# Performance work log

Hardware: AMD Instinct MI355X
Metric: run time of the kernel (lower is better)

## Reference

```python
import jax, jax.numpy as jnp
import numpy as np

B, T, D, H = 4096, 512, 8, 64  # batch, seq_len, input_size, hidden_size


def setup_inputs() -> dict:
    key = jax.random.key(0)
    ks = jax.random.split(key, 11)
    s = lambda k, shape: (jax.random.normal(k, shape, dtype=jnp.float32) * 0.1)
    return {
        "x": jax.random.normal(ks[0], (B, T, D), dtype=jnp.float32),
        # layer 0 (input_size -> H), PyTorch gate order i,f,g,o packed along 4H
        "Wih0": s(ks[1], (4 * H, D)),
        "Whh0": s(ks[2], (4 * H, H)),
        "bih0": s(ks[3], (4 * H,)),
        "bhh0": s(ks[4], (4 * H,)),
        # layer 1 (H -> H)
        "Wih1": s(ks[5], (4 * H, H)),
        "Whh1": s(ks[6], (4 * H, H)),
        "bih1": s(ks[7], (4 * H,)),
        "bhh1": s(ks[8], (4 * H,)),
        # final linear head H -> 1
        "Wfc": s(ks[9], (1, H)),
        "bfc": s(ks[10], (1,)),
    }


def _lstm_layer(x, Wih, Whh, bih, bhh):
    """Single-direction LSTM layer over x:[B,T,Din] -> hs:[B,T,H]."""
    b, t, _ = x.shape
    h_dim = Whh.shape[1]
    # Precompute input contribution for all timesteps (one big GEMM).
    xg = jnp.einsum("btd,gd->btg", x, Wih) + bih + bhh  # [B,T,4H]

    def step(carry, gx_t):
        h, c = carry
        z = gx_t + h @ Whh.T  # [B,4H]
        i, f, g, o = jnp.split(z, 4, axis=-1)
        i = jax.nn.sigmoid(i)
        f = jax.nn.sigmoid(f)
        g = jnp.tanh(g)
        o = jax.nn.sigmoid(o)
        c = f * c + i * g
        h = o * jnp.tanh(c)
        return (h, c), h

    h0 = jnp.zeros((b, h_dim), x.dtype)
    c0 = jnp.zeros((b, h_dim), x.dtype)
    (_, _), hs = jax.lax.scan(step, (h0, c0), jnp.swapaxes(xg, 0, 1))
    return jnp.swapaxes(hs, 0, 1)  # [B,T,H]


def reference(x, Wih0, Whh0, bih0, bhh0, Wih1, Whh1, bih1, bhh1, Wfc, bfc):
    # nn.LSTM with num_layers=2, batch_first=True; dropout inactive in eval.
    h1 = _lstm_layer(x, Wih0, Whh0, bih0, bhh0)
    h2 = _lstm_layer(h1, Wih1, Whh1, bih1, bhh1)
    last = h2[:, -1, :]  # [B,H]
    return last @ Wfc.T + bfc  # [B,1]
```

## Files before the change

kernel.cpp:

```cpp
#include <hip/hip_runtime.h>

#define BTOT 4096
#define TB   512
#define BD   8
#define BSL  16

#define A0P1   2048
#define A1P0   8192
#define A1XOR  4096
#define S0     104
#define S1     136
#define LDSEL  16384

typedef __attribute__((ext_vector_type(8))) short  short8;
typedef __attribute__((ext_vector_type(4))) float  f32x4;

static __device__ __forceinline__ unsigned short f2bf(float f) {
    unsigned u = __float_as_uint(f);
    u += 0x7fffu + ((u >> 16) & 1u);
    return (unsigned short)(u >> 16);
}
static __device__ __forceinline__ float bf2f(unsigned short h) {
    return __uint_as_float(((unsigned)h) << 16);
}
static __device__ __forceinline__ float sigm(float x) {
    float e = __builtin_amdgcn_exp2f(-1.44269504f * x);
    return __builtin_amdgcn_rcpf(1.0f + e);
}
static __device__ __forceinline__ float tanh_(float x) {
    float e = __builtin_amdgcn_exp2f(2.88539008f * x);
    return 1.0f - 2.0f * __builtin_amdgcn_rcpf(1.0f + e);
}

template<int R0>
static __device__ __forceinline__ unsigned gates2(
    const f32x4 ai, const f32x4 af, const f32x4 ag, const f32x4 ao,
    float& c0, float& c1)
{
    float h0, h1;
    {
        const float iv = sigm(ai[R0]),     fv = sigm(af[R0]);
        const float gv = tanh_(ag[R0]),    ov = sigm(ao[R0]);
        c0 = fv * c0 + iv * gv;
        h0 = ov * tanh_(c0);
    }
    {
        const float iv = sigm(ai[R0 + 1]), fv = sigm(af[R0 + 1]);
        const float gv = tanh_(ag[R0 + 1]), ov = sigm(ao[R0 + 1]);
        c1 = fv * c1 + iv * gv;
        h1 = ov * tanh_(c1);
    }
    unsigned hp;
    asm("v_cvt_pk_bf16_f32 %0, %1, %2" : "=v"(hp) : "v"(h0), "v"(h1));
    return hp;
}

__global__ __launch_bounds__(1024) void lstm2_fused(
    const float* __restrict__ x,
    const float* __restrict__ Wih0, const float* __restrict__ Whh0,
    const float* __restrict__ bih0, const float* __restrict__ bhh0,
    const float* __restrict__ Wih1, const float* __restrict__ Whh1,
    const float* __restrict__ bih1, const float* __restrict__ bhh1,
    const float* __restrict__ Wfc,  const float* __restrict__ bfc,
    float* __restrict__ out)
{
    __shared__ __align__(16) unsigned short lds16[LDSEL];

    const int tid  = threadIdx.x;
    const int wid  = tid >> 6;
    const int lane = tid & 63;
    const int q    = lane >> 4;
    const int ln   = lane & 15;
    const int rb   = blockIdx.x * BSL;

    const bool L1w = (wid >= 8);
    const int  w   = L1w ? (wid - 8) : wid;
    const int  g   = w & 3;
    const int  rh  = w >> 2;
    const int  r0  = rh * 2;
    const int  jc  = g * 16 + ln;

    short8 Bf[4][4];
    #pragma unroll
    for (int G = 0; G < 4; ++G) {
        const int n = G * 64 + jc;
        #pragma unroll
        for (int ki = 0; ki < 4; ++ki) {
            union { unsigned short u[8]; short8 v; } t;
            #pragma unroll
            for (int j = 0; j < 8; ++j) {
                const int k = ki * 32 + q * 8 + j;
                float wv = 0.0f;
                if (!L1w) {
                    if (ki < 3) {
                        if (k < 64)      wv = Whh0[n * 64 + k];
                        else if (k < 72) wv = Wih0[n * 8 + (k - 64)];
                    }
                } else {
                    if (k < 64)          wv = Wih1[n * 64 + k];
                    else                 wv = Whh1[n * 64 + (k - 64)];
                }
                t.u[j] = f2bf(wv);
            }
            Bf[G][ki] = t.v;
        }
    }
    float bias[4];
    #pragma unroll
    for (int G = 0; G < 4; ++G) {
        const int n = G * 64 + jc;
        bias[G] = L1w ? (bih1[n] + bhh1[n]) : (bih0[n] + bhh0[n]);
    }

    {
        unsigned* z = (unsigned*)lds16;
        #pragma unroll
        for (int i = 0; i < 8; ++i) z[tid + i * 1024] = 0;
    }
    __syncthreads();

    const int xrow = g * 4 + (lane >> 1), xh = lane & 1;
    if (!L1w && rh == 0 && lane < 8) {
        const float4 v = *(const float4*)(x + ((size_t)(rb + xrow) * TB) * BD + xh * 4);
        unsigned p0, p1;
        asm("v_cvt_pk_bf16_f32 %0, %1, %2" : "=v"(p0) : "v"(v.x), "v"(v.y));
        asm("v_cvt_pk_bf16_f32 %0, %1, %2" : "=v"(p1) : "v"(v.z), "v"(v.w));
        *(uint2*)(lds16 + (xrow * S0 + 64 + xh * 4)) = make_uint2(p0, p1);
    }
    __syncthreads();

    int rdA, wrA, wrC = 0, wrX = 0, xrA, xrW;
    if (!L1w) {
        rdA = ln * S0 + q * 8;
        wrA = A0P1 + (q * 4 + r0) * S0 + jc;
        wrC = A1P0 + (q * 4 + r0) * S1 + jc;
        wrX = A0P1 + xrow * S0 + 64 + xh * 4;
        xrA = A0P1; xrW = A0P1;
    } else {
        rdA = A1P0 + A1XOR + ln * S1 + q * 8;
        wrA = A1P0 + (q * 4 + r0) * S1 + 64 + jc;
        xrA = A1XOR; xrW = A1XOR;
    }

    float cc0 = 0.f, cc1 = 0.f;

    for (int it = 0; it <= TB; ++it) {
        if (!L1w) {
            if (it < TB) {
                float4 xv;
                const bool dox = (rh == 0) && (lane < 8) && (it + 1 < TB);
                if (dox)
                    xv = *(const float4*)(x + ((size_t)(rb + xrow) * TB + (it + 1)) * BD + xh * 4);

                const short8 a0 = *(const short8*)(lds16 + rdA);
                const short8 a1 = *(const short8*)(lds16 + rdA + 32);
                const short8 a2 = *(const short8*)(lds16 + rdA + 64);

                f32x4 ai = {bias[0], bias[0], bias[0], bias[0]};
                f32x4 af = {bias[1], bias[1], bias[1], bias[1]};
                f32x4 ag = {bias[2], bias[2], bias[2], bias[2]};
                f32x4 ao = {bias[3], bias[3], bias[3], bias[3]};
                ai = __builtin_amdgcn_mfma_f32_16x16x32_bf16(a0, Bf[0][0], ai, 0, 0, 0);
                af = __builtin_amdgcn_mfma_f32_16x16x32_bf16(a0, Bf[1][0], af, 0, 0, 0);
                ag = __builtin_amdgcn_mfma_f32_16x16x32_bf16(a0, Bf[2][0], ag, 0, 0, 0);
                ao = __builtin_amdgcn_mfma_f32_16x16x32_bf16(a0, Bf[3][0], ao, 0, 0, 0);
                ai = __builtin_amdgcn_mfma_f32_16x16x32_bf16(a1, Bf[0][1], ai, 0, 0, 0);
                af = __builtin_amdgcn_mfma_f32_16x16x32_bf16(a1, Bf[1][1], af, 0, 0, 0);
                ag = __builtin_amdgcn_mfma_f32_16x16x32_bf16(a1, Bf[2][1], ag, 0, 0, 0);
                ao = __builtin_amdgcn_mfma_f32_16x16x32_bf16(a1, Bf[3][1], ao, 0, 0, 0);
                ai = __builtin_amdgcn_mfma_f32_16x16x32_bf16(a2, Bf[0][2], ai, 0, 0, 0);
                af = __builtin_amdgcn_mfma_f32_16x16x32_bf16(a2, Bf[1][2], af, 0, 0, 0);
                ag = __builtin_amdgcn_mfma_f32_16x16x32_bf16(a2, Bf[2][2], ag, 0, 0, 0);
                ao = __builtin_amdgcn_mfma_f32_16x16x32_bf16(a2, Bf[3][2], ao, 0, 0, 0);

                const unsigned hp = rh ? gates2<2>(ai, af, ag, ao, cc0, cc1)
                                       : gates2<0>(ai, af, ag, ao, cc0, cc1);
                lds16[wrA]      = (unsigned short)hp;
                lds16[wrA + S0] = (unsigned short)(hp >> 16);
                lds16[wrC]      = (unsigned short)hp;
                lds16[wrC + S1] = (unsigned short)(hp >> 16);

                if (dox) {
                    unsigned p0, p1;
                    asm("v_cvt_pk_bf16_f32 %0, %1, %2" : "=v"(p0) : "v"(xv.x), "v"(xv.y));
                    asm("v_cvt_pk_bf16_f32 %0, %1, %2" : "=v"(p1) : "v"(xv.z), "v"(xv.w));
                    *(uint2*)(lds16 + wrX) = make_uint2(p0, p1);
                }
            }
        } else {
            if (it >= 1) {
                const short8 a0 = *(const short8*)(lds16 + rdA);
                const short8 a1 = *(const short8*)(lds16 + rdA + 32);
                const short8 a2 = *(const short8*)(lds16 + rdA + 64);
                const short8 a3 = *(const short8*)(lds16 + rdA + 96);

                f32x4 ai = {bias[0], bias[0], bias[0], bias[0]};
                f32x4 af = {bias[1], bias[1], bias[1], bias[1]};
                f32x4 ag = {bias[2], bias[2], bias[2], bias[2]};
                f32x4 ao = {bias[3], bias[3], bias[3], bias[3]};
                ai = __builtin_amdgcn_mfma_f32_16x16x32_bf16(a0, Bf[0][0], ai, 0, 0, 0);
                af = __builtin_amdgcn_mfma_f32_16x16x32_bf16(a0, Bf[1][0], af, 0, 0, 0);
                ag = __builtin_amdgcn_mfma_f32_16x16x32_bf16(a0, Bf[2][0], ag, 0, 0, 0);
                ao = __builtin_amdgcn_mfma_f32_16x16x32_bf16(a0, Bf[3][0], ao, 0, 0, 0);
                ai = __builtin_amdgcn_mfma_f32_16x16x32_bf16(a1, Bf[0][1], ai, 0, 0, 0);
                af = __builtin_amdgcn_mfma_f32_16x16x32_bf16(a1, Bf[1][1], af, 0, 0, 0);
                ag = __builtin_amdgcn_mfma_f32_16x16x32_bf16(a1, Bf[2][1], ag, 0, 0, 0);
                ao = __builtin_amdgcn_mfma_f32_16x16x32_bf16(a1, Bf[3][1], ao, 0, 0, 0);
                ai = __builtin_amdgcn_mfma_f32_16x16x32_bf16(a2, Bf[0][2], ai, 0, 0, 0);
                af = __builtin_amdgcn_mfma_f32_16x16x32_bf16(a2, Bf[1][2], af, 0, 0, 0);
                ag = __builtin_amdgcn_mfma_f32_16x16x32_bf16(a2, Bf[2][2], ag, 0, 0, 0);
                ao = __builtin_amdgcn_mfma_f32_16x16x32_bf16(a2, Bf[3][2], ao, 0, 0, 0);
                ai = __builtin_amdgcn_mfma_f32_16x16x32_bf16(a3, Bf[0][3], ai, 0, 0, 0);
                af = __builtin_amdgcn_mfma_f32_16x16x32_bf16(a3, Bf[1][3], af, 0, 0, 0);
                ag = __builtin_amdgcn_mfma_f32_16x16x32_bf16(a3, Bf[2][3], ag, 0, 0, 0);
                ao = __builtin_amdgcn_mfma_f32_16x16x32_bf16(a3, Bf[3][3], ao, 0, 0, 0);

                const unsigned hp = rh ? gates2<2>(ai, af, ag, ao, cc0, cc1)
                                       : gates2<0>(ai, af, ag, ao, cc0, cc1);
                lds16[wrA]      = (unsigned short)hp;
                lds16[wrA + S1] = (unsigned short)(hp >> 16);
            }
        }
        __syncthreads();
        rdA ^= xrA; wrA ^= xrW; wrC ^= A1XOR; wrX ^= A0P1;
    }

    if (tid < BSL) {
        float s = bfc[0];
        #pragma unroll 8
        for (int j = 0; j < 64; ++j)
            s += bf2f(lds16[A1P0 + tid * S1 + 64 + j]) * Wfc[j];
        out[rb + tid] = s;
    }
}

extern "C" void kernel_launch(void* const* d_in, const int* in_sizes, int n_in,
                              void* d_out, int out_size, void* d_ws, size_t ws_size,
                              hipStream_t stream) {
    const float* x    = (const float*)d_in[0];
    const float* Wih0 = (const float*)d_in[1];
    const float* Whh0 = (const float*)d_in[2];
    const float* bih0 = (const float*)d_in[3];
    const float* bhh0 = (const float*)d_in[4];
    const float* Wih1 = (const float*)d_in[5];
    const float* Whh1 = (const float*)d_in[6];
    const float* bih1 = (const float*)d_in[7];
    const float* bhh1 = (const float*)d_in[8];
    const float* Wfc  = (const float*)d_in[9];
    const float* bfc  = (const float*)d_in[10];
    float* out = (float*)d_out;

    dim3 grid(BTOT / BSL);
    dim3 block(1024);
    lstm2_fused<<<grid, block, 0, stream>>>(x, Wih0, Whh0, bih0, bhh0,
                                            Wih1, Whh1, bih1, bhh1, Wfc, bfc, out);
}
```

Baseline: 607.5 us.

## Halve block to 512 threads, batch gate transcendentals, restage x and h layout

Each wave now covers all four accumulator rows, so a block uses 8 waves instead of 16 and two blocks can share a CU. The sigmoid and tanh scale factors are folded into the bf16 weights and biases. Reciprocals are batched with a product-tree trick so each row group needs one rcp instead of many. x is staged into LDS in 64-step chunks with wide coalesced loads, replacing per-step global loads. The h buffers get a new k-major layout, and the duplicate write of layer-0 h into a separate layer-1 buffer is removed. The batched reciprocal trades accuracy and overflow safety for fewer transcendental ops.

```diff
diff --git a/kernel.cpp b/kernel.cpp
--- a/kernel.cpp
+++ b/kernel.cpp
@@ -5,12 +5,12 @@
 #define BD   8
 #define BSL  16
 
-#define A0P1   2048
-#define A1P0   8192
-#define A1XOR  4096
-#define S0     104
-#define S1     136
-#define LDSEL  16384
+#define A0TOG  2048
+#define A1BASE 4096
+#define A1TOG  1024
+#define XBASE  6144
+#define XTOG   8192
+#define NLDS   22528
 
 typedef __attribute__((ext_vector_type(8))) short  short8;
 typedef __attribute__((ext_vector_type(4))) float  f32x4;
@@ -23,39 +23,86 @@
 static __device__ __forceinline__ float bf2f(unsigned short h) {
     return __uint_as_float(((unsigned)h) << 16);
 }
-static __device__ __forceinline__ float sigm(float x) {
-    float e = __builtin_amdgcn_exp2f(-1.44269504f * x);
-    return __builtin_amdgcn_rcpf(1.0f + e);
-}
-static __device__ __forceinline__ float tanh_(float x) {
-    float e = __builtin_amdgcn_exp2f(2.88539008f * x);
-    return 1.0f - 2.0f * __builtin_amdgcn_rcpf(1.0f + e);
-}
-
-template<int R0>
-static __device__ __forceinline__ unsigned gates2(
+static __device__ __forceinline__ unsigned pkbf(float a, float b) {
+    unsigned r;
+    asm("v_cvt_pk_bf16_f32 %0, %1, %2" : "=v"(r) : "v"(a), "v"(b));
+    return r;
+}
+
+static __device__ __forceinline__ void inv8(const float d[8], float v[8]) {
+    const float p0 = d[0]*d[1], p1 = d[2]*d[3], p2 = d[4]*d[5], p3 = d[6]*d[7];
+    const float q0 = p0*p1, q1 = p2*p3;
+    const float r  = __builtin_amdgcn_rcpf(q0*q1);
+    const float iq0 = q1*r,  iq1 = q0*r;
+    const float ip0 = p1*iq0, ip1 = p0*iq0, ip2 = p3*iq1, ip3 = p2*iq1;
+    v[0]=d[1]*ip0; v[1]=d[0]*ip0; v[2]=d[3]*ip1; v[3]=d[2]*ip1;
+    v[4]=d[5]*ip2; v[5]=d[4]*ip2; v[6]=d[7]*ip3; v[7]=d[6]*ip3;
+}
+static __device__ __forceinline__ void inv4(const float d[4], float v[4]) {
+    const float p0 = d[0]*d[1], p1 = d[2]*d[3];
+    const float r  = __builtin_amdgcn_rcpf(p0*p1);
+    const float ip0 = p1*r, ip1 = p0*r;
+    v[0]=d[1]*ip0; v[1]=d[0]*ip0; v[2]=d[3]*ip1; v[3]=d[2]*ip1;
+}
+
+static __device__ __forceinline__ void gates4(
     const f32x4 ai, const f32x4 af, const f32x4 ag, const f32x4 ao,
-    float& c0, float& c1)
+    float cc[4], unsigned hp[2])
 {
-    float h0, h1;
-    {
-        const float iv = sigm(ai[R0]),     fv = sigm(af[R0]);
-        const float gv = tanh_(ag[R0]),    ov = sigm(ao[R0]);
-        c0 = fv * c0 + iv * gv;
-        h0 = ov * tanh_(c0);
-    }
-    {
-        const float iv = sigm(ai[R0 + 1]), fv = sigm(af[R0 + 1]);
-        const float gv = tanh_(ag[R0 + 1]), ov = sigm(ao[R0 + 1]);
-        c1 = fv * c1 + iv * gv;
-        h1 = ov * tanh_(c1);
-    }
-    unsigned hp;
-    asm("v_cvt_pk_bf16_f32 %0, %1, %2" : "=v"(hp) : "v"(h0), "v"(h1));
-    return hp;
-}
-
-__global__ __launch_bounds__(1024) void lstm2_fused(
+    float ei[4], ef[4], eg[4], eo[4];
+    #pragma unroll
+    for (int r = 0; r < 4; ++r) {
+        ei[r] = __builtin_amdgcn_exp2f(ai[r]);
+        ef[r] = __builtin_amdgcn_exp2f(af[r]);
+        eg[r] = __builtin_amdgcn_exp2f(ag[r]);
+        eo[r] = __builtin_amdgcn_exp2f(ao[r]);
+    }
+    const float d01[8] = {1.f+ei[0],1.f+ef[0],1.f+eg[0],1.f+eo[0],
+                          1.f+ei[1],1.f+ef[1],1.f+eg[1],1.f+eo[1]};
+    const float d23[8] = {1.f+ei[2],1.f+ef[2],1.f+eg[2],1.f+eo[2],
+                          1.f+ei[3],1.f+ef[3],1.f+eg[3],1.f+eo[3]};
+    float v01[8], v23[8];
+    inv8(d01, v01); inv8(d23, v23);
+    const float iv[4] = {v01[0], v01[4], v23[0], v23[4]};
+    const float fv[4] = {v01[1], v01[5], v23[1], v23[5]};
+    const float gd[4] = {v01[2], v01[6], v23[2], v23[6]};
+    const float ov[4] = {v01[3], v01[7], v23[3], v23[7]};
+    float nc[4], dc[4];
+    #pragma unroll
+    for (int r = 0; r < 4; ++r) {
+        const float gv = (eg[r] - 1.f) * gd[r];
+        cc[r] = fv[r] * cc[r] + iv[r] * gv;
+        const float ec = __builtin_amdgcn_exp2f(2.88539008f * cc[r]);
+        nc[r] = ec - 1.f; dc[r] = ec + 1.f;
+    }
+    float id[4];
+    inv4(dc, id);
+    const float h0 = ov[0]*(nc[0]*id[0]), h1 = ov[1]*(nc[1]*id[1]);
+    const float h2 = ov[2]*(nc[2]*id[2]), h3 = ov[3]*(nc[3]*id[3]);
+    hp[0] = pkbf(h0, h1); hp[1] = pkbf(h2, h3);
+}
+
+static __device__ __forceinline__ void stage_x(
+    unsigned short* lds16, const float* __restrict__ x, int rb, int tid, int t0)
+{
+    const int buf = (t0 >> 6) & 1;
+    const int row = tid >> 5, u = tid & 31;
+    const float* gp = x + (size_t)(rb + row) * (TB * BD) + t0 * BD + u * 16;
+    const float4 v0 = ((const float4*)gp)[0];
+    const float4 v1 = ((const float4*)gp)[1];
+    const float4 v2 = ((const float4*)gp)[2];
+    const float4 v3 = ((const float4*)gp)[3];
+    const int el = XBASE + buf * XTOG + (u * 2) * 128 + row * 8;
+    uint4 s0, s1;
+    s0.x = pkbf(v0.x, v0.y); s0.y = pkbf(v0.z, v0.w);
+    s0.z = pkbf(v1.x, v1.y); s0.w = pkbf(v1.z, v1.w);
+    s1.x = pkbf(v2.x, v2.y); s1.y = pkbf(v2.z, v2.w);
+    s1.z = pkbf(v3.x, v3.y); s1.w = pkbf(v3.z, v3.w);
+    *(uint4*)(lds16 + el)       = s0;
+    *(uint4*)(lds16 + el + 128) = s1;
+}
+
+__global__ __launch_bounds__(512, 2) void lstm2_fused(
     const float* __restrict__ x,
     const float* __restrict__ Wih0, const float* __restrict__ Whh0,
     const float* __restrict__ bih0, const float* __restrict__ bhh0,
@@ -64,7 +111,7 @@
     const float* __restrict__ Wfc,  const float* __restrict__ bfc,
     float* __restrict__ out)
 {
-    __shared__ __align__(16) unsigned short lds16[LDSEL];
+    __shared__ __align__(16) unsigned short lds16[NLDS];
 
     const int tid  = threadIdx.x;
     const int wid  = tid >> 6;
@@ -73,17 +120,17 @@
     const int ln   = lane & 15;
     const int rb   = blockIdx.x * BSL;
 
-    const bool L1w = (wid >= 8);
-    const int  w   = L1w ? (wid - 8) : wid;
-    const int  g   = w & 3;
-    const int  rh  = w >> 2;
-    const int  r0  = rh * 2;
+    const bool L1w = (wid >= 4);
+    const int  g   = L1w ? (wid - 4) : wid;
     const int  jc  = g * 16 + ln;
 
+    const float SCI = -1.44269504f;
+    const float SCG =  2.88539008f;
     short8 Bf[4][4];
     #pragma unroll
     for (int G = 0; G < 4; ++G) {
         const int n = G * 64 + jc;
+        const float sc = (G == 2) ? SCG : SCI;
         #pragma unroll
         for (int ki = 0; ki < 4; ++ki) {
             union { unsigned short u[8]; short8 v; } t;
@@ -100,7 +147,7 @@
                     if (k < 64)          wv = Wih1[n * 64 + k];
                     else                 wv = Whh1[n * 64 + (k - 64)];
                 }
-                t.u[j] = f2bf(wv);
+                t.u[j] = f2bf(sc * wv);
             }
             Bf[G][ki] = t.v;
         }
@@ -109,52 +156,49 @@
     #pragma unroll
     for (int G = 0; G < 4; ++G) {
         const int n = G * 64 + jc;
-        bias[G] = L1w ? (bih1[n] + bhh1[n]) : (bih0[n] + bhh0[n]);
-    }
-
+        const float sc = (G == 2) ? SCG : SCI;
+        bias[G] = sc * (L1w ? (bih1[n] + bhh1[n]) : (bih0[n] + bhh0[n]));
+    }
+
+    stage_x(lds16, x, rb, tid, 0);
     {
         unsigned* z = (unsigned*)lds16;
         #pragma unroll
-        for (int i = 0; i < 8; ++i) z[tid + i * 1024] = 0;
+        for (int i = 0; i < 6; ++i) z[tid + i * 512] = 0;
     }
     __syncthreads();
-
-    const int xrow = g * 4 + (lane >> 1), xh = lane & 1;
-    if (!L1w && rh == 0 && lane < 8) {
-        const float4 v = *(const float4*)(x + ((size_t)(rb + xrow) * TB) * BD + xh * 4);
-        unsigned p0, p1;
-        asm("v_cvt_pk_bf16_f32 %0, %1, %2" : "=v"(p0) : "v"(v.x), "v"(v.y));
-        asm("v_cvt_pk_bf16_f32 %0, %1, %2" : "=v"(p1) : "v"(v.z), "v"(v.w));
-        *(uint2*)(lds16 + (xrow * S0 + 64 + xh * 4)) = make_uint2(p0, p1);
+    if (tid < 16) {
+        const uint4 v = *(const uint4*)(lds16 + XBASE + tid * 8);
+        *(uint4*)(lds16 + 8 * 128 + tid * 8) = v;
     }
     __syncthreads();
 
-    int rdA, wrA, wrC = 0, wrX = 0, xrA, xrW;
-    if (!L1w) {
-        rdA = ln * S0 + q * 8;
-        wrA = A0P1 + (q * 4 + r0) * S0 + jc;
-        wrC = A1P0 + (q * 4 + r0) * S1 + jc;
-        wrX = A0P1 + xrow * S0 + 64 + xh * 4;
-        xrA = A0P1; xrW = A0P1;
-    } else {
-        rdA = A1P0 + A1XOR + ln * S1 + q * 8;
-        wrA = A1P0 + (q * 4 + r0) * S1 + 64 + jc;
-        xrA = A1XOR; xrW = A1XOR;
-    }
-
-    float cc0 = 0.f, cc1 = 0.f;
+    const int rbase = q * 128 + ln * 8;
+    const int wb    = (jc >> 3) * 128 + q * 32 + (jc & 7);
+    int rdA  = rbase;
+    int wr0  = A0TOG + wb;
+    int rdH0 = rbase;
+    int rdH1 = A1BASE + rbase;
+    int wrH1 = A1BASE + A1TOG + wb;
+    int xw   = A0TOG + 1024 + lane * 8;
+
+    float cc[4] = {0.f, 0.f, 0.f, 0.f};
 
     for (int it = 0; it <= TB; ++it) {
+        if (((it & 63) == 62) && (it + 2 < TB))
+            stage_x(lds16, x, rb, tid, it + 2);
+
         if (!L1w) {
             if (it < TB) {
-                float4 xv;
-                const bool dox = (rh == 0) && (lane < 8) && (it + 1 < TB);
-                if (dox)
-                    xv = *(const float4*)(x + ((size_t)(rb + xrow) * TB + (it + 1)) * BD + xh * 4);
-
+                if (wid == 0 && lane < 16 && it + 1 < TB) {
+                    const int tn = it + 1;
+                    const int xr = XBASE + ((tn >> 6) & 1) * XTOG + (tn & 63) * 128 + lane * 8;
+                    const uint4 v = *(const uint4*)(lds16 + xr);
+                    *(uint4*)(lds16 + xw) = v;
+                }
                 const short8 a0 = *(const short8*)(lds16 + rdA);
-                const short8 a1 = *(const short8*)(lds16 + rdA + 32);
-                const short8 a2 = *(const short8*)(lds16 + rdA + 64);
+                const short8 a1 = *(const short8*)(lds16 + rdA + 512);
+                const short8 a2 = *(const short8*)(lds16 + rdA + 1024);
 
                 f32x4 ai = {bias[0], bias[0], bias[0], bias[0]};
                 f32x4 af = {bias[1], bias[1], bias[1], bias[1]};
@@ -173,26 +217,19 @@
                 ag = __builtin_amdgcn_mfma_f32_16x16x32_bf16(a2, Bf[2][2], ag, 0, 0, 0);
                 ao = __builtin_amdgcn_mfma_f32_16x16x32_bf16(a2, Bf[3][2], ao, 0, 0, 0);
 
-                const unsigned hp = rh ? gates2<2>(ai, af, ag, ao, cc0, cc1)
-                                       : gates2<0>(ai, af, ag, ao, cc0, cc1);
-                lds16[wrA]      = (unsigned short)hp;
-                lds16[wrA + S0] = (unsigned short)(hp >> 16);
-                lds16[wrC]      = (unsigned short)hp;
-                lds16[wrC + S1] = (unsigned short)(hp >> 16);
-
-                if (dox) {
-                    unsigned p0, p1;
-                    asm("v_cvt_pk_bf16_f32 %0, %1, %2" : "=v"(p0) : "v"(xv.x), "v"(xv.y));
-                    asm("v_cvt_pk_bf16_f32 %0, %1, %2" : "=v"(p1) : "v"(xv.z), "v"(xv.w));
-                    *(uint2*)(lds16 + wrX) = make_uint2(p0, p1);
-                }
+                unsigned hp[2];
+                gates4(ai, af, ag, ao, cc, hp);
+                lds16[wr0]           = (unsigned short)hp[0];
+                lds16[wr0 + 8]       = (unsigned short)(hp[0] >> 16);
+                lds16[wr0 + 16]      = (unsigned short)hp[1];
+                lds16[wr0 + 24]      = (unsigned short)(hp[1] >> 16);
             }
         } else {
             if (it >= 1) {
-                const short8 a0 = *(const short8*)(lds16 + rdA);
-                const short8 a1 = *(const short8*)(lds16 + rdA + 32);
-                const short8 a2 = *(const short8*)(lds16 + rdA + 64);
-                const short8 a3 = *(const short8*)(lds16 + rdA + 96);
+                const short8 a0 = *(const short8*)(lds16 + rdH0);
+                const short8 a1 = *(const short8*)(lds16 + rdH0 + 512);
+                const short8 a2 = *(const short8*)(lds16 + rdH1);
+                const short8 a3 = *(const short8*)(lds16 + rdH1 + 512);
 
                 f32x4 ai = {bias[0], bias[0], bias[0], bias[0]};
                 f32x4 af = {bias[1], bias[1], bias[1], bias[1]};
@@ -215,21 +252,24 @@
                 ag = __builtin_amdgcn_mfma_f32_16x16x32_bf16(a3, Bf[2][3], ag, 0, 0, 0);
                 ao = __builtin_amdgcn_mfma_f32_16x16x32_bf16(a3, Bf[3][3], ao, 0, 0, 0);
 
-                const unsigned hp = rh ? gates2<2>(ai, af, ag, ao, cc0, cc1)
-                                       : gates2<0>(ai, af, ag, ao, cc0, cc1);
-                lds16[wrA]      = (unsigned short)hp;
-                lds16[wrA + S1] = (unsigned short)(hp >> 16);
+                unsigned hp[2];
+                gates4(ai, af, ag, ao, cc, hp);
+                lds16[wrH1]          = (unsigned short)hp[0];
+                lds16[wrH1 + 8]      = (unsigned short)(hp[0] >> 16);
+                lds16[wrH1 + 16]     = (unsigned short)hp[1];
+                lds16[wrH1 + 24]     = (unsigned short)(hp[1] >> 16);
             }
         }
         __syncthreads();
-        rdA ^= xrA; wrA ^= xrW; wrC ^= A1XOR; wrX ^= A0P1;
+        rdA ^= A0TOG; wr0 ^= A0TOG; rdH0 ^= A0TOG; xw ^= A0TOG;
+        rdH1 ^= A1TOG; wrH1 ^= A1TOG;
     }
 
     if (tid < BSL) {
         float s = bfc[0];
         #pragma unroll 8
         for (int j = 0; j < 64; ++j)
-            s += bf2f(lds16[A1P0 + tid * S1 + 64 + j]) * Wfc[j];
+            s += bf2f(lds16[A1BASE + A1TOG + (j >> 3) * 128 + tid * 8 + (j & 7)]) * Wfc[j];
         out[rb + tid] = s;
     }
 }
@@ -251,7 +291,7 @@
     float* out = (float*)d_out;
 
     dim3 grid(BTOT / BSL);
-    dim3 block(1024);
+    dim3 block(512);
     lstm2_fused<<<grid, block, 0, stream>>>(x, Wih0, Whh0, bih0, bhh0,
                                             Wih1, Whh1, bih1, bhh1, Wfc, bfc, out);
 }
```

After: 604.7 us. Within noise of the previous version (-0.5%).
